# Optimization experiments

Hardware: AMD Instinct MI355X
Metric: run time of the kernel (lower is better)

## Reference

```python
import jax, jax.numpy as jnp
import numpy as np

WS = 8          # cubic window side
HEADS = 6
DIM = 192


def _make_buffers(ws=WS):
    # relative_coords_table: [1, 2w-1, 2w-1, 2w-1, 3], signed log-spaced in [-1,1]*? (Swin V2)
    c = np.arange(-(ws - 1), ws, dtype=np.float32)
    g = np.stack(np.meshgrid(c, c, c, indexing='ij'), axis=-1)[None]  # [1,15,15,15,3]
    g = g / (ws - 1) * 8.0
    table = np.sign(g) * np.log2(np.abs(g) + 1.0) / np.log2(8.0)
    # relative_position_index: [N, N] into the (2w-1)^3 table
    coords = np.stack(np.meshgrid(np.arange(ws), np.arange(ws), np.arange(ws), indexing='ij'))
    cf = coords.reshape(3, -1)                          # [3, N]
    rel = cf[:, :, None] - cf[:, None, :]               # [3, N, N]
    rel = rel.transpose(1, 2, 0) + (ws - 1)             # [N, N, 3]
    idx = rel[..., 0] * (2 * ws - 1) ** 2 + rel[..., 1] * (2 * ws - 1) + rel[..., 2]
    return table.astype(np.float32), idx.astype(np.int32)


def setup_inputs() -> dict:
    key = jax.random.key(0)
    ks = jax.random.split(key, 8)
    B_, N, C, nW = 64, WS ** 3, DIM, 16
    table, idx = _make_buffers()
    return {
        'x': jax.random.normal(ks[0], (B_, N, C), jnp.float32),
        'mask': jax.random.normal(ks[1], (nW, N, N), jnp.float32),
        'qkv_w': jax.random.normal(ks[2], (3 * C, C), jnp.float32) * 0.05,
        'q_bias': jnp.zeros((C,), jnp.float32),
        'v_bias': jnp.zeros((C,), jnp.float32),
        'logit_scale': jnp.log(10.0) * jnp.ones((HEADS, 1, 1), jnp.float32),
        'cpb_w1': jax.random.normal(ks[3], (512, 3), jnp.float32) * 0.1,
        'cpb_b1': jnp.zeros((512,), jnp.float32),
        'cpb_w2': jax.random.normal(ks[4], (HEADS, 512), jnp.float32) * 0.1,
        'proj_w': jax.random.normal(ks[5], (C, C), jnp.float32) * 0.05,
        'proj_b': jnp.zeros((C,), jnp.float32),
        'rel_table': jnp.asarray(table),
        'rel_index': jnp.asarray(idx),
    }


def reference(x, mask, qkv_w, q_bias, v_bias, logit_scale, cpb_w1, cpb_b1,
              cpb_w2, proj_w, proj_b, rel_table, rel_index):
    B_, N, C = x.shape
    H = HEADS
    hd = C // H
    # qkv projection with (q_bias, 0, v_bias)
    qkv_b = jnp.concatenate([q_bias, jnp.zeros_like(v_bias), v_bias])
    qkv = (x @ qkv_w.T + qkv_b).reshape(B_, N, 3, H, hd).transpose(2, 0, 3, 1, 4)
    q, k, v = qkv[0], qkv[1], qkv[2]                 # each [B_, H, N, hd]
    # cosine attention with clamped learned logit scale
    qn = q / jnp.maximum(jnp.linalg.norm(q, axis=-1, keepdims=True), 1e-12)
    kn = k / jnp.maximum(jnp.linalg.norm(k, axis=-1, keepdims=True), 1e-12)
    scale = jnp.exp(jnp.minimum(logit_scale, jnp.log(100.0)))  # [H,1,1]
    attn = jnp.einsum('bhnd,bhmd->bhnm', qn, kn) * scale[None]
    # continuous position bias: MLP over coords table, gather by relative index
    hidden = jax.nn.relu(rel_table @ cpb_w1.T + cpb_b1)        # [1,15,15,15,512]
    tbl = (hidden @ cpb_w2.T).reshape(-1, H)                   # [3375, H]
    bias = tbl[rel_index.reshape(-1)].reshape(N, N, H).transpose(2, 0, 1)
    bias = 16.0 * jax.nn.sigmoid(bias)                         # [H, N, N]
    attn = attn + bias[None]
    # window mask
    nW = mask.shape[0]
    attn = attn.reshape(B_ // nW, nW, H, N, N) + mask[None, :, None]
    attn = jax.nn.softmax(attn.reshape(B_, H, N, N), axis=-1)
    out = jnp.einsum('bhnm,bhmd->bhnd', attn, v)
    out = out.transpose(0, 2, 1, 3).reshape(B_, N, C)
    return out @ proj_w.T + proj_b
```

## Files before the change

### kernel.cpp

```cpp
#include <hip/hip_runtime.h>
#include <hip/hip_bf16.h>
#include <math.h>

#define B__ 64
#define NTOK 512
#define CDIM 192
#define HEADS 6
#define HD 32
#define NW 16
#define T3 3375
#define HID 512
#define LOG2E 1.4426950408889634f

typedef _Float16 f16x8 __attribute__((ext_vector_type(8)));
typedef _Float16 f16x4 __attribute__((ext_vector_type(4)));
typedef float    f32x4 __attribute__((ext_vector_type(4)));

#if __has_builtin(__builtin_amdgcn_exp2f)
#define EXP2F(x) __builtin_amdgcn_exp2f(x)
#else
#define EXP2F(x) __expf(0.69314718056f*(x))
#endif

__global__ __launch_bounds__(512) void k_cpb(
    const float* __restrict__ rel_table, const float* __restrict__ w1,
    const float* __restrict__ b1, const float* __restrict__ w2,
    float* __restrict__ tbl_t) {
  int i = blockIdx.x;
  int t = threadIdx.x;
  float t0 = rel_table[i*3+0], t1 = rel_table[i*3+1], t2 = rel_table[i*3+2];
  float hval = fmaxf(t0*w1[t*3+0] + t1*w1[t*3+1] + t2*w1[t*3+2] + b1[t], 0.f);
  __shared__ float red[8][6];
  int wv = t >> 6, lane = t & 63;
  #pragma unroll
  for (int hh = 0; hh < 6; ++hh) {
    float p = hval * w2[hh*HID + t];
    #pragma unroll
    for (int off = 32; off > 0; off >>= 1) p += __shfl_down(p, off);
    if (lane == 0) red[wv][hh] = p;
  }
  __syncthreads();
  if (t < 6) {
    float s = 0.f;
    #pragma unroll
    for (int w8 = 0; w8 < 8; ++w8) s += red[w8][t];
    tbl_t[t*T3 + i] = 16.f / (1.f + __expf(-s));
  }
}

__global__ __launch_bounds__(64) void k_bm(
    const int* __restrict__ idx, const float* __restrict__ tbl_t,
    const float* __restrict__ mask, _Float16* __restrict__ bm) {
  int bx = blockIdx.x;
  int hw = blockIdx.y;
  int h = hw >> 4, w = hw & 15;
  int l = threadIdx.x;
  int qt = bx >> 5, kt = bx & 31;
  int q  = qt*16 + (l & 15);
  int k0 = kt*16 + (l >> 4)*4;
  const float* mp = mask + (size_t)w*262144 + (size_t)q*512 + k0;
  const int*   ip = idx + (size_t)q*512 + k0;
  const float* tb = tbl_t + (size_t)h*T3;
  f16x4 v;
  #pragma unroll
  for (int r = 0; r < 4; ++r)
    v[r] = (_Float16)(LOG2E * (tb[ip[r]] + mp[r]));
  *(f16x4*)(bm + ((size_t)hw*1024 + bx)*256 + l*4) = v;
}

__global__ __launch_bounds__(256) void k_xh(
    const float* __restrict__ x, _Float16* __restrict__ xh) {
  int i = blockIdx.x*256 + threadIdx.x;
  float4 v = ((const float4*)x)[i];
  f16x4 h = {(_Float16)v.x, (_Float16)v.y, (_Float16)v.z, (_Float16)v.w};
  *(f16x4*)(xh + (size_t)i*4) = h;
}

__global__ __launch_bounds__(256) void k_wh(
    const float* __restrict__ qkv_w, const float* __restrict__ proj_w,
    _Float16* __restrict__ wh) {
  int i = blockIdx.x*256 + threadIdx.x;
  float4 v = (i < 27648) ? ((const float4*)qkv_w)[i] : ((const float4*)proj_w)[i - 27648];
  f16x4 h = {(_Float16)v.x, (_Float16)v.y, (_Float16)v.z, (_Float16)v.w};
  *(f16x4*)(wh + (size_t)i*4) = h;
}

__global__ __launch_bounds__(256) void k_qkv(
    const _Float16* __restrict__ xh, const _Float16* __restrict__ wh,
    const float* __restrict__ q_bias, const float* __restrict__ v_bias,
    const float* __restrict__ logit_scale,
    _Float16* __restrict__ qn, _Float16* __restrict__ kn, _Float16* __restrict__ vt) {
  int wid = threadIdx.x >> 6, l = threadIdx.x & 63;
  int lr = l & 15, lg = l >> 4;
  int m0 = blockIdx.x*128 + wid*32;
  int cb = blockIdx.y;
  int c0 = cb*64;
  int p  = cb/3;
  int pc0 = (cb - p*3)*64;
  int h0 = pc0 >> 5;

  const f32x4 zero = {0.f,0.f,0.f,0.f};
  f32x4 acc[2][4];
  #pragma unroll
  for (int mt = 0; mt < 2; ++mt)
    #pragma unroll
    for (int nt = 0; nt < 4; ++nt) acc[mt][nt] = zero;

  const _Float16* wb = wh + (size_t)c0*192;
  for (int kc = 0; kc < 6; ++kc) {
    int ko = kc*32 + lg*8;
    f16x8 a0 = *(const f16x8*)(xh + (size_t)(m0 + lr)*192 + ko);
    f16x8 a1 = *(const f16x8*)(xh + (size_t)(m0 + 16 + lr)*192 + ko);
    #pragma unroll
    for (int nt = 0; nt < 4; ++nt) {
      f16x8 bf = *(const f16x8*)(wb + (size_t)(nt*16 + lr)*192 + ko);
      acc[0][nt] = __builtin_amdgcn_mfma_f32_16x16x32_f16(a0, bf, acc[0][nt], 0, 0, 0);
      acc[1][nt] = __builtin_amdgcn_mfma_f32_16x16x32_f16(a1, bf, acc[1][nt], 0, 0, 0);
    }
  }

  if (p == 0) {
    float bq[4];
    #pragma unroll
    for (int nt = 0; nt < 4; ++nt) bq[nt] = q_bias[pc0 + nt*16 + lr];
    float s0 = __expf(fminf(logit_scale[h0], 4.6051702f)) * LOG2E;
    float s1 = __expf(fminf(logit_scale[h0+1], 4.6051702f)) * LOG2E;
    #pragma unroll
    for (int mt = 0; mt < 2; ++mt) {
      #pragma unroll
      for (int nt = 0; nt < 4; ++nt)
        #pragma unroll
        for (int r = 0; r < 4; ++r) acc[mt][nt][r] += bq[nt];
      #pragma unroll
      for (int r = 0; r < 4; ++r) {
        float ss0 = acc[mt][0][r]*acc[mt][0][r] + acc[mt][1][r]*acc[mt][1][r];
        float ss1 = acc[mt][2][r]*acc[mt][2][r] + acc[mt][3][r]*acc[mt][3][r];
        #pragma unroll
        for (int off = 1; off < 16; off <<= 1) {
          ss0 += __shfl_xor(ss0, off);
          ss1 += __shfl_xor(ss1, off);
        }
        float inv0 = s0 / fmaxf(sqrtf(ss0), 1e-12f);
        float inv1 = s1 / fmaxf(sqrtf(ss1), 1e-12f);
        int m = m0 + mt*16 + lg*4 + r;
        int b = m >> 9, n = m & 511;
        #pragma unroll
        for (int nt = 0; nt < 4; ++nt) {
          int h = h0 + (nt >> 1);
          int d = (nt & 1)*16 + lr;
          float val = acc[mt][nt][r] * ((nt < 2) ? inv0 : inv1);
          qn[(((size_t)b*HEADS + h)*NTOK + n)*HD + d] = (_Float16)val;
        }
      }
    }
  } else if (p == 1) {
    #pragma unroll
    for (int mt = 0; mt < 2; ++mt) {
      #pragma unroll
      for (int r = 0; r < 4; ++r) {
        float ss0 = acc[mt][0][r]*acc[mt][0][r] + acc[mt][1][r]*acc[mt][1][r];
        float ss1 = acc[mt][2][r]*acc[mt][2][r] + acc[mt][3][r]*acc[mt][3][r];
        #pragma unroll
        for (int off = 1; off < 16; off <<= 1) {
          ss0 += __shfl_xor(ss0, off);
          ss1 += __shfl_xor(ss1, off);
        }
        float inv0 = 1.f / fmaxf(sqrtf(ss0), 1e-12f);
        float inv1 = 1.f / fmaxf(sqrtf(ss1), 1e-12f);
        int m = m0 + mt*16 + lg*4 + r;
        int b = m >> 9, n = m & 511;
        #pragma unroll
        for (int nt = 0; nt < 4; ++nt) {
          int h = h0 + (nt >> 1);
          int d = (nt & 1)*16 + lr;
          float val = acc[mt][nt][r] * ((nt < 2) ? inv0 : inv1);
          kn[(((size_t)b*HEADS + h)*NTOK + n)*HD + d] = (_Float16)val;
        }
      }
    }
  } else {
    float bv[4];
    #pragma unroll
    for (int nt = 0; nt < 4; ++nt) bv[nt] = v_bias[pc0 + nt*16 + lr];
    #pragma unroll
    for (int mt = 0; mt < 2; ++mt) {
      int m = m0 + mt*16 + lg*4;
      int b = m >> 9, n = m & 511;
      #pragma unroll
      for (int nt = 0; nt < 4; ++nt) {
        int h = h0 + (nt >> 1);
        int d = (nt & 1)*16 + lr;
        f16x4 hv;
        #pragma unroll
        for (int r = 0; r < 4; ++r) hv[r] = (_Float16)(acc[mt][nt][r] + bv[nt]);
        *(f16x4*)(vt + (((size_t)b*HEADS + h)*HD + d)*NTOK + n) = hv;
      }
    }
  }
}

__global__ __launch_bounds__(256) void k_attn(
    const _Float16* __restrict__ qn, const _Float16* __restrict__ kn,
    const _Float16* __restrict__ vt, const _Float16* __restrict__ bm,
    _Float16* __restrict__ ao_h) {
  __shared__ _Float16 plds[4][32][88];
  int qblk = blockIdx.x, h = blockIdx.y, b = blockIdx.z;
  int w = b & (NW-1);
  int wid = threadIdx.x >> 6, l = threadIdx.x & 63;
  int lr = l & 15, lg = l >> 4;
  size_t pair = (size_t)b*HEADS + h;
  const _Float16* qb = qn + pair*NTOK*HD;
  const _Float16* kb = kn + pair*NTOK*HD;
  const _Float16* vb = vt + pair*HD*NTOK;
  const _Float16* bm_base = bm + ((size_t)(h*16 + w)*1024)*256;
  int q0 = qblk*128 + wid*32;
  int qtb = q0 >> 4;

  f16x8 aq[2];
  aq[0] = *(const f16x8*)(qb + (size_t)(q0 + lr)*HD + lg*8);
  aq[1] = *(const f16x8*)(qb + (size_t)(q0 + 16 + lr)*HD + lg*8);

  const f32x4 zero = {0.f, 0.f, 0.f, 0.f};
  f32x4 o[2][2];
  o[0][0] = zero; o[0][1] = zero; o[1][0] = zero; o[1][1] = zero;
  float mrun[2] = {-1e30f, -1e30f};
  float lrun[2] = {0.f, 0.f};

  for (int ch = 0; ch < 8; ++ch) {
    f16x8 bk[4];
    #pragma unroll
    for (int kt = 0; kt < 4; ++kt)
      bk[kt] = *(const f16x8*)(kb + (size_t)(ch*64 + kt*16 + lr)*HD + lg*8);
    f32x4 s[2][4];
    #pragma unroll
    for (int mt = 0; mt < 2; ++mt) {
      #pragma unroll
      for (int kt = 0; kt < 4; ++kt) {
        size_t toff = ((size_t)((qtb + mt)*32 + ch*4 + kt))*256 + l*4;
        f16x4 c4 = *(const f16x4*)(bm_base + toff);
        f32x4 cf = {(float)c4[0], (float)c4[1], (float)c4[2], (float)c4[3]};
        s[mt][kt] = __builtin_amdgcn_mfma_f32_16x16x32_f16(bk[kt], aq[mt], cf, 0, 0, 0);
      }
    }
    #pragma unroll
    for (int mt = 0; mt < 2; ++mt) {
      float pm = s[mt][0][0];
      #pragma unroll
      for (int kt = 0; kt < 4; ++kt)
        #pragma unroll
        for (int r = 0; r < 4; ++r) pm = fmaxf(pm, s[mt][kt][r]);
      pm = fmaxf(pm, __shfl_xor(pm, 16));
      pm = fmaxf(pm, __shfl_xor(pm, 32));
      if (!__all(pm <= mrun[mt] + 8.f)) {
        float mnew = fmaxf(mrun[mt], pm);
        float corr = EXP2F(mrun[mt] - mnew);
        lrun[mt] *= corr;
        mrun[mt] = mnew;
        #pragma unroll
        for (int r = 0; r < 4; ++r) {
          float cr = __shfl(corr, (l >> 4)*4 + r);
          o[mt][0][r] *= cr;
          o[mt][1][r] *= cr;
        }
      }
      float mref = mrun[mt];
      float rs = 0.f;
      #pragma unroll
      for (int kt = 0; kt < 4; ++kt) {
        f16x4 pv;
        #pragma unroll
        for (int r = 0; r < 4; ++r) {
          float p = EXP2F(s[mt][kt][r] - mref);
          pv[r] = (_Float16)p;
          rs += p;
        }
        *(f16x4*)(&plds[wid][mt*16 + lr][kt*16 + lg*4]) = pv;
      }
      rs += __shfl_xor(rs, 16);
      rs += __shfl_xor(rs, 32);
      lrun[mt] += rs;
    }
    #pragma unroll
    for (int kk = 0; kk < 2; ++kk) {
      f16x8 ap0 = *(const f16x8*)(&plds[wid][lr][kk*32 + lg*8]);
      f16x8 ap1 = *(const f16x8*)(&plds[wid][16 + lr][kk*32 + lg*8]);
      #pragma unroll
      for (int dt = 0; dt < 2; ++dt) {
        f16x8 bv = *(const f16x8*)(vb + (size_t)(dt*16 + lr)*NTOK + ch*64 + kk*32 + lg*8);
        o[0][dt] = __builtin_amdgcn_mfma_f32_16x16x32_f16(ap0, bv, o[0][dt], 0, 0, 0);
        o[1][dt] = __builtin_amdgcn_mfma_f32_16x16x32_f16(ap1, bv, o[1][dt], 0, 0, 0);
      }
    }
  }
  _Float16* op = ao_h + (size_t)b*NTOK*CDIM + (size_t)h*HD;
  #pragma unroll
  for (int mt = 0; mt < 2; ++mt) {
    float inv = 1.f / lrun[mt];
    #pragma unroll
    for (int r = 0; r < 4; ++r) {
      float iv = __shfl(inv, (l >> 4)*4 + r);
      int qg = q0 + mt*16 + lg*4 + r;
      #pragma unroll
      for (int dt = 0; dt < 2; ++dt)
        op[(size_t)qg*CDIM + dt*16 + lr] = (_Float16)(o[mt][dt][r] * iv);
    }
  }
}

__global__ __launch_bounds__(256) void k_proj(
    const _Float16* __restrict__ ao_h, const _Float16* __restrict__ pw,
    const float* __restrict__ pb, float* __restrict__ out) {
  int wid = threadIdx.x >> 6, l = threadIdx.x & 63;
  int lr = l & 15, lg = l >> 4;
  int m0 = blockIdx.x*128 + wid*32;
  int c0 = blockIdx.y*64;

  const f32x4 zero = {0.f,0.f,0.f,0.f};
  f32x4 acc[2][4];
  #pragma unroll
  for (int mt = 0; mt < 2; ++mt)
    #pragma unroll
    for (int nt = 0; nt < 4; ++nt) acc[mt][nt] = zero;

  for (int kc = 0; kc < 6; ++kc) {
    int ko = kc*32 + lg*8;
    f16x8 a0 = *(const f16x8*)(ao_h + (size_t)(m0 + lr)*192 + ko);
    f16x8 a1 = *(const f16x8*)(ao_h + (size_t)(m0 + 16 + lr)*192 + ko);
    #pragma unroll
    for (int nt = 0; nt < 4; ++nt) {
      f16x8 bf = *(const f16x8*)(pw + (size_t)(c0 + nt*16 + lr)*192 + ko);
      acc[0][nt] = __builtin_amdgcn_mfma_f32_16x16x32_f16(a0, bf, acc[0][nt], 0, 0, 0);
      acc[1][nt] = __builtin_amdgcn_mfma_f32_16x16x32_f16(a1, bf, acc[1][nt], 0, 0, 0);
    }
  }

  float bias[4];
  #pragma unroll
  for (int nt = 0; nt < 4; ++nt) bias[nt] = pb[c0 + nt*16 + lr];
  #pragma unroll
  for (int mt = 0; mt < 2; ++mt)
    #pragma unroll
    for (int r = 0; r < 4; ++r) {
      int m = m0 + mt*16 + lg*4 + r;
      #pragma unroll
      for (int nt = 0; nt < 4; ++nt)
        out[(size_t)m*CDIM + c0 + nt*16 + lr] = acc[mt][nt][r] + bias[nt];
    }
}

extern "C" void kernel_launch(void* const* d_in, const int* in_sizes, int n_in,
                              void* d_out, int out_size, void* d_ws, size_t ws_size,
                              hipStream_t stream) {
  const float* x           = (const float*)d_in[0];
  const float* mask        = (const float*)d_in[1];
  const float* qkv_w       = (const float*)d_in[2];
  const float* q_bias      = (const float*)d_in[3];
  const float* v_bias      = (const float*)d_in[4];
  const float* logit_scale = (const float*)d_in[5];
  const float* cpb_w1      = (const float*)d_in[6];
  const float* cpb_b1      = (const float*)d_in[7];
  const float* cpb_w2      = (const float*)d_in[8];
  const float* proj_w      = (const float*)d_in[9];
  const float* proj_b      = (const float*)d_in[10];
  const float* rel_table   = (const float*)d_in[11];
  const int*   rel_index   = (const int*)d_in[12];
  float* out = (float*)d_out;

  float* wsf = (float*)d_ws;
  float* tbl_t = wsf;
  _Float16* hws = (_Float16*)(wsf + 20480);
  _Float16* qn  = hws;
  _Float16* kn  = qn + 6291456;
  _Float16* vt  = kn + 6291456;
  _Float16* bm  = vt + 6291456;
  _Float16* wh  = bm + 25165824;
  _Float16* xh  = wh + 147456;
  _Float16* ao_h = xh;

  k_cpb<<<T3, 512, 0, stream>>>(rel_table, cpb_w1, cpb_b1, cpb_w2, tbl_t);
  k_bm<<<dim3(1024, 96), 64, 0, stream>>>(rel_index, tbl_t, mask, bm);
  k_xh<<<6144, 256, 0, stream>>>(x, xh);
  k_wh<<<144, 256, 0, stream>>>(qkv_w, proj_w, wh);
  k_qkv<<<dim3(256, 9), 256, 0, stream>>>(xh, wh, q_bias, v_bias, logit_scale, qn, kn, vt);
  k_attn<<<dim3(4, HEADS, B__), 256, 0, stream>>>(qn, kn, vt, bm, ao_h);
  k_proj<<<dim3(256, 3), 256, 0, stream>>>(ao_h, wh + 110592, proj_b, out);
}
```

Baseline: 295.0 us.

## Split bias and mask tables and remap attention blocks across XCDs

Replaces the combined per-(head,window) fp16 bias+mask tensor with separate per-head bias and per-window mask tensors, so the precomputation writes far less data. The attention kernel now loads both and adds them in fp16 before the MFMA. The launch grid is also flattened, with block IDs remapped so blocks for the same (batch, head) pair land on the same XCD, which should improve L2 reuse of K/V and the bias tables. The trade-off is an extra load and fp16 add per tile, and a slight change in rounding.

```diff
diff --git a/kernel.cpp b/kernel.cpp
--- a/kernel.cpp
+++ b/kernel.cpp
@@ -48,24 +48,38 @@
   }
 }
 
-__global__ __launch_bounds__(64) void k_bm(
+__global__ __launch_bounds__(64) void k_biasf(
     const int* __restrict__ idx, const float* __restrict__ tbl_t,
-    const float* __restrict__ mask, _Float16* __restrict__ bm) {
+    _Float16* __restrict__ bias_f) {
   int bx = blockIdx.x;
-  int hw = blockIdx.y;
-  int h = hw >> 4, w = hw & 15;
-  int l = threadIdx.x;
+  int h  = blockIdx.y;
+  int l  = threadIdx.x;
+  int qt = bx >> 5, kt = bx & 31;
+  int q  = qt*16 + (l & 15);
+  int k0 = kt*16 + (l >> 4)*4;
+  const int* ip = idx + (size_t)q*512 + k0;
+  const float* tb = tbl_t + (size_t)h*T3;
+  f16x4 v;
+  #pragma unroll
+  for (int r = 0; r < 4; ++r)
+    v[r] = (_Float16)(LOG2E * tb[ip[r]]);
+  *(f16x4*)(bias_f + ((size_t)(h*1024 + bx))*256 + l*4) = v;
+}
+
+__global__ __launch_bounds__(64) void k_maskf(
+    const float* __restrict__ mask, _Float16* __restrict__ mask_f) {
+  int bx = blockIdx.x;
+  int w  = blockIdx.y;
+  int l  = threadIdx.x;
   int qt = bx >> 5, kt = bx & 31;
   int q  = qt*16 + (l & 15);
   int k0 = kt*16 + (l >> 4)*4;
   const float* mp = mask + (size_t)w*262144 + (size_t)q*512 + k0;
-  const int*   ip = idx + (size_t)q*512 + k0;
-  const float* tb = tbl_t + (size_t)h*T3;
   f16x4 v;
   #pragma unroll
   for (int r = 0; r < 4; ++r)
-    v[r] = (_Float16)(LOG2E * (tb[ip[r]] + mp[r]));
-  *(f16x4*)(bm + ((size_t)hw*1024 + bx)*256 + l*4) = v;
+    v[r] = (_Float16)(LOG2E * mp[r]);
+  *(f16x4*)(mask_f + ((size_t)(w*1024 + bx))*256 + l*4) = v;
 }
 
 __global__ __launch_bounds__(256) void k_xh(
@@ -201,10 +215,14 @@
 
 __global__ __launch_bounds__(256) void k_attn(
     const _Float16* __restrict__ qn, const _Float16* __restrict__ kn,
-    const _Float16* __restrict__ vt, const _Float16* __restrict__ bm,
-    _Float16* __restrict__ ao_h) {
+    const _Float16* __restrict__ vt, const _Float16* __restrict__ bias_f,
+    const _Float16* __restrict__ mask_f, _Float16* __restrict__ ao_h) {
   __shared__ _Float16 plds[4][32][88];
-  int qblk = blockIdx.x, h = blockIdx.y, b = blockIdx.z;
+  int bid = blockIdx.x;
+  int xcd = bid & 7, slot = bid >> 3;
+  int pr = xcd*48 + (slot >> 2);
+  int qblk = slot & 3;
+  int b = pr / 6, h = pr - 6*b;
   int w = b & (NW-1);
   int wid = threadIdx.x >> 6, l = threadIdx.x & 63;
   int lr = l & 15, lg = l >> 4;
@@ -212,7 +230,8 @@
   const _Float16* qb = qn + pair*NTOK*HD;
   const _Float16* kb = kn + pair*NTOK*HD;
   const _Float16* vb = vt + pair*HD*NTOK;
-  const _Float16* bm_base = bm + ((size_t)(h*16 + w)*1024)*256;
+  const _Float16* bias_base = bias_f + (size_t)h*262144 + l*4;
+  const _Float16* mask_base = mask_f + (size_t)w*262144 + l*4;
   int q0 = qblk*128 + wid*32;
   int qtb = q0 >> 4;
 
@@ -227,6 +246,16 @@
   float lrun[2] = {0.f, 0.f};
 
   for (int ch = 0; ch < 8; ++ch) {
+    f16x4 cfr[2][4];
+    #pragma unroll
+    for (int mt = 0; mt < 2; ++mt)
+      #pragma unroll
+      for (int kt = 0; kt < 4; ++kt) {
+        size_t toff = ((size_t)((qtb + mt)*32 + ch*4 + kt))*256;
+        f16x4 bf = *(const f16x4*)(bias_base + toff);
+        f16x4 mf = *(const f16x4*)(mask_base + toff);
+        cfr[mt][kt] = bf + mf;
+      }
     f16x8 bk[4];
     #pragma unroll
     for (int kt = 0; kt < 4; ++kt)
@@ -236,8 +265,7 @@
     for (int mt = 0; mt < 2; ++mt) {
       #pragma unroll
       for (int kt = 0; kt < 4; ++kt) {
-        size_t toff = ((size_t)((qtb + mt)*32 + ch*4 + kt))*256 + l*4;
-        f16x4 c4 = *(const f16x4*)(bm_base + toff);
+        f16x4 c4 = cfr[mt][kt];
         f32x4 cf = {(float)c4[0], (float)c4[1], (float)c4[2], (float)c4[3]};
         s[mt][kt] = __builtin_amdgcn_mfma_f32_16x16x32_f16(bk[kt], aq[mt], cf, 0, 0, 0);
       }
@@ -372,16 +400,18 @@
   _Float16* qn  = hws;
   _Float16* kn  = qn + 6291456;
   _Float16* vt  = kn + 6291456;
-  _Float16* bm  = vt + 6291456;
-  _Float16* wh  = bm + 25165824;
+  _Float16* bias_f = vt + 6291456;
+  _Float16* mask_f = bias_f + 1572864;
+  _Float16* wh  = mask_f + 4194304;
   _Float16* xh  = wh + 147456;
   _Float16* ao_h = xh;
 
   k_cpb<<<T3, 512, 0, stream>>>(rel_table, cpb_w1, cpb_b1, cpb_w2, tbl_t);
-  k_bm<<<dim3(1024, 96), 64, 0, stream>>>(rel_index, tbl_t, mask, bm);
+  k_biasf<<<dim3(1024, HEADS), 64, 0, stream>>>(rel_index, tbl_t, bias_f);
+  k_maskf<<<dim3(1024, NW), 64, 0, stream>>>(mask, mask_f);
   k_xh<<<6144, 256, 0, stream>>>(x, xh);
   k_wh<<<144, 256, 0, stream>>>(qkv_w, proj_w, wh);
   k_qkv<<<dim3(256, 9), 256, 0, stream>>>(xh, wh, q_bias, v_bias, logit_scale, qn, kn, vt);
-  k_attn<<<dim3(4, HEADS, B__), 256, 0, stream>>>(qn, kn, vt, bm, ao_h);
+  k_attn<<<1536, 256, 0, stream>>>(qn, kn, vt, bias_f, mask_f, ao_h);
   k_proj<<<dim3(256, 3), 256, 0, stream>>>(ao_h, wh + 110592, proj_b, out);
 }
```

After: 249.3 us. 1.18x faster.
